# Kernel tuning notes

Measured on AMD Instinct MI355X. Metric: run time of the kernel, lower is better.

Reference implementation:

```python
import jax, jax.numpy as jnp
import numpy as np

N = 20000
E = 320000
F_IN = 256
HID = 32
HEADS = 8
EDGE_DIM = HID // 4  # 8
NEG_SLOPE = 0.2


def _gat_conv(x, src, dst, e_emb, W, att_s, att_d, W_e, att_e, bias, H, C):
    """PyG-style GATConv with edge_dim, add_self_loops=True (fill_value='mean'), concat heads."""
    n = x.shape[0]
    loop = jnp.arange(n, dtype=src.dtype)
    # self-loop edge_attr = scatter-mean of edge_attr by dst (0 for isolated nodes)
    deg = jax.ops.segment_sum(jnp.ones_like(dst, dtype=x.dtype), dst, num_segments=n)
    e_mean = jax.ops.segment_sum(e_emb, dst, num_segments=n) / jnp.maximum(deg, 1.0)[:, None]
    src_a = jnp.concatenate([src, loop])
    dst_a = jnp.concatenate([dst, loop])
    e_all = jnp.concatenate([e_emb, e_mean], axis=0)  # [E+N, edge_dim]

    h = (x @ W).reshape(n, H, C)                      # [N,H,C]
    a_src = jnp.einsum('nhc,hc->nh', h, att_s)        # [N,H]
    a_dst = jnp.einsum('nhc,hc->nh', h, att_d)
    he = (e_all @ W_e).reshape(-1, H, C)              # [E+N,H,C]
    a_edge = jnp.einsum('ehc,hc->eh', he, att_e)      # [E+N,H]

    alpha = jax.nn.leaky_relu(a_src[src_a] + a_dst[dst_a] + a_edge, NEG_SLOPE)
    # segment softmax over destination nodes
    amax = jax.ops.segment_max(alpha, dst_a, num_segments=n)
    alpha = jnp.exp(alpha - amax[dst_a])
    denom = jax.ops.segment_sum(alpha, dst_a, num_segments=n)
    alpha = alpha / (denom[dst_a] + 1e-16)

    msg = h[src_a] * alpha[:, :, None]                # [E+N,H,C]
    out = jax.ops.segment_sum(msg, dst_a, num_segments=n)  # [N,H,C]
    return out.reshape(n, H * C) + bias


def setup_inputs() -> dict:
    key = jax.random.key(0)
    ks = jax.random.split(key, 16)

    def glorot(k, shape):
        fan_in, fan_out = shape[0], shape[-1]
        s = np.sqrt(6.0 / (fan_in + fan_out))
        return jax.random.uniform(k, shape, jnp.float32, -s, s)

    x = jax.random.normal(ks[0], (N, F_IN), jnp.float32)
    edge_index = jax.random.randint(ks[1], (2, E), 0, N, jnp.int32)
    edge_attr = jax.random.uniform(ks[2], (E, 2), jnp.float32)

    # spatial_embed: Linear(2 -> EDGE_DIM)
    Wse = glorot(ks[3], (2, EDGE_DIM))
    bse = jnp.zeros((EDGE_DIM,), jnp.float32)
    # conv1: in=F_IN, heads=HEADS, out=HID, edge_dim=EDGE_DIM
    W1 = glorot(ks[4], (F_IN, HEADS * HID))
    as1 = glorot(ks[5], (HEADS, HID))
    ad1 = glorot(ks[6], (HEADS, HID))
    We1 = glorot(ks[7], (EDGE_DIM, HEADS * HID))
    ae1 = glorot(ks[8], (HEADS, HID))
    b1 = jnp.zeros((HEADS * HID,), jnp.float32)
    # conv2: in=HEADS*HID, heads=1, out=HID
    W2 = glorot(ks[9], (HEADS * HID, HID))
    as2 = glorot(ks[10], (1, HID))
    ad2 = glorot(ks[11], (1, HID))
    We2 = glorot(ks[12], (EDGE_DIM, HID))
    ae2 = glorot(ks[13], (1, HID))
    b2 = jnp.zeros((HID,), jnp.float32)

    return {"x": x, "edge_index": edge_index, "edge_attr": edge_attr,
            "Wse": Wse, "bse": bse,
            "W1": W1, "as1": as1, "ad1": ad1, "We1": We1, "ae1": ae1, "b1": b1,
            "W2": W2, "as2": as2, "ad2": ad2, "We2": We2, "ae2": ae2, "b2": b2}


def reference(x, edge_index, edge_attr, Wse, bse,
              W1, as1, ad1, We1, ae1, b1,
              W2, as2, ad2, We2, ae2, b2):
    src, dst = edge_index[0], edge_index[1]
    e = jax.nn.relu(edge_attr @ Wse + bse)            # [E, EDGE_DIM]
    h = _gat_conv(x, src, dst, e, W1, as1, ad1, We1, ae1, b1, HEADS, HID)
    h = jax.nn.relu(h)                                # dropout inactive (eval)
    out = _gat_conv(h, src, dst, e, W2, as2, ad2, We2, ae2, b2, 1, HID)
    return out
```

## Files before the change

### kernel.cpp

```cpp
#include <hip/hip_runtime.h>
#include <hip/hip_bf16.h>
#include <hip/hip_fp16.h>
#include <float.h>


typedef short v8s __attribute__((ext_vector_type(8)));
typedef float v4f __attribute__((ext_vector_type(4)));

#define WSYNC() do { __asm__ volatile("" ::: "memory"); __builtin_amdgcn_wave_barrier(); } while (0)

__device__ __forceinline__ ushort f2bf(float f) {
  unsigned u = __float_as_uint(f);
  u = (u + 0x7FFF + ((u >> 16) & 1)) >> 16;
  return (ushort)u;
}
__device__ __forceinline__ float bf2f(ushort h) {
  return __uint_as_float(((unsigned)h) << 16);
}
__device__ __forceinline__ unsigned pk2bf(float lo, float hi) {
  return (unsigned)f2bf(lo) | ((unsigned)f2bf(hi) << 16);
}
__device__ __forceinline__ unsigned pk2h(float lo, float hi) {
  return (unsigned)__half_as_ushort(__float2half(lo)) |
         ((unsigned)__half_as_ushort(__float2half(hi)) << 16);
}

__global__ __launch_bounds__(256) void k_pre(const int* __restrict__ dst,
                                             const float* __restrict__ W1,
                                             const float* __restrict__ We1,
                                             const float* __restrict__ ae1,
                                             const float* __restrict__ We2,
                                             const float* __restrict__ ae2,
                                             const float* __restrict__ W2,
                                             int* __restrict__ deg,
                                             ushort* __restrict__ Bt,
                                             float* __restrict__ M1,
                                             float* __restrict__ m2,
                                             float* __restrict__ W2B,
                                             int E, int DB) {
  int b = blockIdx.x;
  if (b < DB) {
    int e = b * 256 + threadIdx.x;
    if (e < E) atomicAdd(&deg[dst[e]], 1);
    return;
  }
  if (b == DB + 64) {
    int t = threadIdx.x;
    for (int i = t; i < 8192; i += 256) {
      int k = i >> 5, cc = i & 31;
      W2B[(size_t)(k >> 2) * 128 + cc * 4 + (k & 3)] = W2[(size_t)k * 32 + cc];
    }
    if (t < 64) {
      int k = t >> 3, h = t & 7;
      float s = 0.f;
      for (int c = 0; c < 32; c++) s += We1[k * 256 + h * 32 + c] * ae1[h * 32 + c];
      M1[k * 8 + h] = s;
    } else if (t < 72) {
      int k = t - 64;
      float s = 0.f;
      for (int c = 0; c < 32; c++) s += We2[k * 32 + c] * ae2[c];
      m2[k] = s;
    }
    return;
  }
  int b2 = b - DB;
  __shared__ float tile[32][33];
  int bx = b2 & 7, by = b2 >> 3;
  int tx = threadIdx.x & 31, ty = threadIdx.x >> 5;
  for (int r = ty; r < 32; r += 8)
    tile[r][tx] = W1[(size_t)(by * 32 + r) * 256 + bx * 32 + tx];
  __syncthreads();
  for (int r = ty; r < 32; r += 8)
    Bt[(size_t)(bx * 32 + r) * 256 + by * 32 + tx] = f2bf(tile[tx][r]);
}

__global__ __launch_bounds__(1024) void k_scan(const int* __restrict__ deg,
                                               int* __restrict__ row_ptr,
                                               int* __restrict__ cursor, int N) {
  __shared__ int part[1024];
  int tid = threadIdx.x;
  int chunk = (N + 1023) / 1024;
  int lo = tid * chunk;
  if (lo > N) lo = N;
  int hi = lo + chunk;
  if (hi > N) hi = N;
  int s = 0;
  for (int i = lo; i < hi; i++) { s += deg[i]; cursor[i] = 0; }
  part[tid] = s;
  __syncthreads();
  for (int off = 1; off < 1024; off <<= 1) {
    int v = 0;
    if (tid >= off) v = part[tid - off];
    __syncthreads();
    part[tid] += v;
    __syncthreads();
  }
  int base = part[tid] - s;
  for (int i = lo; i < hi; i++) { row_ptr[i] = base; base += deg[i]; }
  if (tid == 1023) row_ptr[N] = part[1023];
}

__global__ __launch_bounds__(256) void k_mega1(
    const float* __restrict__ A, const ushort* __restrict__ Bt,
    const float* __restrict__ as1, const float* __restrict__ ad1,
    ushort* __restrict__ h1b, float* __restrict__ asv, float* __restrict__ adv, int M,
    const int* __restrict__ src, const int* __restrict__ dst,
    const float* __restrict__ ea, const float* __restrict__ Wse,
    const float* __restrict__ bse, const float* __restrict__ M1,
    const float* __restrict__ m2, const int* __restrict__ row_ptr,
    int* __restrict__ cursor, char* __restrict__ rec, int E, int GB) {
  __shared__ __align__(16) char smem[27648];
  int t = threadIdx.x;
  if (blockIdx.x >= GB) {
    float* sW  = (float*)smem;
    float* sbv = sW + 16;
    float* sM  = sbv + 8;
    float* sm2 = sM + 64;
    if (t < 16) sW[t] = Wse[t];
    if (t < 8) sbv[t] = bse[t];
    if (t < 64) sM[t] = M1[t];
    if (t >= 64 && t < 72) sm2[t - 64] = m2[t - 64];
    __syncthreads();
    int i = (blockIdx.x - GB) * 256 + t;
    if (i >= E) return;
    float2 av = ((const float2*)ea)[i];
    float e8[8];
#pragma unroll
    for (int k = 0; k < 8; k++)
      e8[k] = fmaxf(av.x * sW[k] + av.y * sW[8 + k] + sbv[k], 0.f);
    float o[8];
#pragma unroll
    for (int h = 0; h < 8; h++) {
      float s = 0.f;
#pragma unroll
      for (int k = 0; k < 8; k++) s += e8[k] * sM[k * 8 + h];
      o[h] = s;
    }
    float s2 = 0.f;
#pragma unroll
    for (int k = 0; k < 8; k++) s2 += e8[k] * sm2[k];
    int d = dst[i];
    int pos = row_ptr[d] + atomicAdd(&cursor[d], 1);
    uint4 w0, w1;
    w0.x = (unsigned)src[i];
    w0.y = pk2h(o[0], o[1]);
    w0.z = pk2h(o[2], o[3]);
    w0.w = pk2h(o[4], o[5]);
    w1.x = pk2h(o[6], o[7]);
    w1.y = __float_as_uint(s2);
    w1.z = 0; w1.w = 0;
    *(uint4*)(rec + (size_t)pos * 32)      = w0;
    *(uint4*)(rec + (size_t)pos * 32 + 16) = w1;
    return;
  }
  ushort* sA = (ushort*)smem;
  ushort* sB = (ushort*)(smem + 5120);
  float* sas = (float*)(smem + 25600);
  float* sad = (float*)(smem + 26624);
  int wave = t >> 6, lane = t & 63;
  int m0 = blockIdx.x * 64;
  int c = lane & 15, kg = lane >> 4;
  sas[t] = as1[t];
  sad[t] = ad1[t];
  v4f acc[4][4];
#pragma unroll
  for (int a = 0; a < 4; a++)
#pragma unroll
    for (int b = 0; b < 4; b++) acc[a][b] = (v4f)(0.f);
  int arow = t >> 2;
  int akoff = (t & 3) * 8;
  bool aval = (m0 + arow) < M;
  const float* aptr = A + (size_t)(m0 + arow) * 256 + akoff;
  const ushort* bptr = Bt + (size_t)t * 256;
  for (int k0 = 0; k0 < 256; k0 += 32) {
    float4 v0 = make_float4(0.f, 0.f, 0.f, 0.f), v1 = v0;
    if (aval) { v0 = *(const float4*)(aptr + k0); v1 = *(const float4*)(aptr + k0 + 4); }
    unsigned* dst32 = (unsigned*)&sA[arow * 40 + akoff];
    dst32[0] = pk2bf(v0.x, v0.y);
    dst32[1] = pk2bf(v0.z, v0.w);
    dst32[2] = pk2bf(v1.x, v1.y);
    dst32[3] = pk2bf(v1.z, v1.w);
    *(v8s*)&sB[t * 40 + 0]  = *(const v8s*)(bptr + k0 + 0);
    *(v8s*)&sB[t * 40 + 8]  = *(const v8s*)(bptr + k0 + 8);
    *(v8s*)&sB[t * 40 + 16] = *(const v8s*)(bptr + k0 + 16);
    *(v8s*)&sB[t * 40 + 24] = *(const v8s*)(bptr + k0 + 24);
    __syncthreads();
    v8s af[4], bfr[4];
#pragma unroll
    for (int mt = 0; mt < 4; mt++) af[mt] = *(v8s*)&sA[(mt * 16 + c) * 40 + kg * 8];
#pragma unroll
    for (int nt = 0; nt < 4; nt++) bfr[nt] = *(v8s*)&sB[(wave * 64 + nt * 16 + c) * 40 + kg * 8];
#pragma unroll
    for (int mt = 0; mt < 4; mt++)
#pragma unroll
      for (int nt = 0; nt < 4; nt++)
        acc[mt][nt] = __builtin_amdgcn_mfma_f32_16x16x32_bf16(af[mt], bfr[nt], acc[mt][nt], 0, 0, 0);
    __syncthreads();
  }
  int colbase = wave * 64;
#pragma unroll
  for (int mt = 0; mt < 4; mt++) {
#pragma unroll
    for (int i = 0; i < 4; i++) {
      int m = m0 + mt * 16 + kg * 4 + i;
      if (m < M) {
#pragma unroll
        for (int nt = 0; nt < 4; nt++)
          h1b[(size_t)m * 256 + colbase + nt * 16 + c] = f2bf(acc[mt][nt][i]);
      }
      float s1a = acc[mt][0][i] * sas[colbase + c]      + acc[mt][1][i] * sas[colbase + 16 + c];
      float s2a = acc[mt][0][i] * sad[colbase + c]      + acc[mt][1][i] * sad[colbase + 16 + c];
      float s1b = acc[mt][2][i] * sas[colbase + 32 + c] + acc[mt][3][i] * sas[colbase + 48 + c];
      float s2b = acc[mt][2][i] * sad[colbase + 32 + c] + acc[mt][3][i] * sad[colbase + 48 + c];
#pragma unroll
      for (int o = 1; o < 16; o <<= 1) {
        s1a += __shfl_xor(s1a, o);
        s2a += __shfl_xor(s2a, o);
        s1b += __shfl_xor(s1b, o);
        s2b += __shfl_xor(s2b, o);
      }
      if (c == 0 && m < M) {
        asv[(size_t)m * 8 + 2 * wave]     = s1a;
        adv[(size_t)m * 8 + 2 * wave]     = s2a;
        asv[(size_t)m * 8 + 2 * wave + 1] = s1b;
        adv[(size_t)m * 8 + 2 * wave + 1] = s2b;
      }
    }
  }
}

__global__ __launch_bounds__(256) void k_conv1(
    const int* __restrict__ row_ptr, const char* __restrict__ rec,
    const float* __restrict__ asv, const float* __restrict__ adv,
    const ushort* __restrict__ h1b, const float* __restrict__ b1,
    const float* __restrict__ W2B, const float* __restrict__ as2,
    const float* __restrict__ ad2, float* __restrict__ g2,
    float* __restrict__ asv2, float* __restrict__ adv2, int N) {
  __shared__ float sw_all[4][64 * 8];
  __shared__ int ssrc_all[4][64];
  __shared__ float sm_all[4][8], sl_all[4][8], sadv_all[4][8], smean_all[4][8];
  __shared__ float sh2_all[4][256];
  int wid = threadIdx.x >> 6;
  int lane = threadIdx.x & 63;
  int n = blockIdx.x * 4 + wid;
  if (n >= N) return;
  float* sw = sw_all[wid];
  int* ssrc = ssrc_all[wid];
  float* sm = sm_all[wid];
  float* sl = sl_all[wid];
  float* sadv = sadv_all[wid];
  float* smean = smean_all[wid];
  float* sh2 = sh2_all[wid];
  int h = lane >> 3;
  int sub = lane & 7;
  int hh = lane & 7;
  int begin = row_ptr[n], end = row_ptr[n + 1];
  int degr = end - begin;
  if (lane < 8) { sm[lane] = -FLT_MAX; sl[lane] = 0.f; sadv[lane] = adv[(size_t)n * 8 + lane]; }
  WSYNC();
  float aedsum = 0.f;
  float4 acc = make_float4(0.f, 0.f, 0.f, 0.f);
  for (int cs = begin; cs < end; cs += 64) {
    int c = min(64, end - cs);
    WSYNC();
    if (lane < c) ssrc[lane] = *(const int*)(rec + (size_t)(cs + lane) * 32);
    WSYNC();
    for (int idx = lane; idx < c * 8; idx += 64) {
      int el = idx >> 3;
      float ae = __half2float(*(const __half*)(rec + (size_t)(cs + el) * 32 + 4 + hh * 2));
      aedsum += ae;
      float a = asv[(size_t)ssrc[el] * 8 + hh] + sadv[hh] + ae;
      a = a > 0.f ? a : 0.2f * a;
      sw[idx] = a;
    }
    WSYNC();
    float mloc = -FLT_MAX;
    for (int el = sub; el < c; el += 8) mloc = fmaxf(mloc, sw[el * 8 + h]);
#pragma unroll
    for (int o = 1; o < 8; o <<= 1) mloc = fmaxf(mloc, __shfl_xor(mloc, o));
    float mold = sm[h];
    float mnew = fmaxf(mold, mloc);
    float scale = __expf(mold - mnew);
    float lloc = 0.f;
    for (int el = sub; el < c; el += 8) {
      float w = __expf(sw[el * 8 + h] - mnew);
      sw[el * 8 + h] = w;
      lloc += w;
    }
#pragma unroll
    for (int o = 1; o < 8; o <<= 1) lloc += __shfl_xor(lloc, o);
    WSYNC();
    if (sub == 0) { sm[h] = mnew; sl[h] = sl[h] * scale + lloc; }
    acc.x *= scale; acc.y *= scale; acc.z *= scale; acc.w *= scale;
#pragma unroll 2
    for (int el = 0; el < c; el++) {
      float w = sw[el * 8 + h];
      ushort4 hv = *(const ushort4*)(h1b + (size_t)ssrc[el] * 256 + lane * 4);
      acc.x += w * bf2f(hv.x);
      acc.y += w * bf2f(hv.y);
      acc.z += w * bf2f(hv.z);
      acc.w += w * bf2f(hv.w);
    }
  }
  aedsum += __shfl_xor(aedsum, 8);
  aedsum += __shfl_xor(aedsum, 16);
  aedsum += __shfl_xor(aedsum, 32);
  float invd = 1.f / (float)(degr > 1 ? degr : 1);
  if (lane < 8) smean[lane] = aedsum * invd;
  WSYNC();
  float a_self = asv[(size_t)n * 8 + h] + sadv[h] + smean[h];
  a_self = a_self > 0.f ? a_self : 0.2f * a_self;
  float mold = sm[h];
  float mnew = fmaxf(mold, a_self);
  float scale = __expf(mold - mnew);
  float w_self = __expf(a_self - mnew);
  float l_fin = sl[h] * scale + w_self;
  ushort4 hs = *(const ushort4*)(h1b + (size_t)n * 256 + lane * 4);
  acc.x = acc.x * scale + w_self * bf2f(hs.x);
  acc.y = acc.y * scale + w_self * bf2f(hs.y);
  acc.z = acc.z * scale + w_self * bf2f(hs.z);
  acc.w = acc.w * scale + w_self * bf2f(hs.w);
  float inv = 1.f / (l_fin + 1e-16f);
  float4 bv = *(const float4*)(b1 + lane * 4);
  float4 h2v;
  h2v.x = fmaxf(acc.x * inv + bv.x, 0.f);
  h2v.y = fmaxf(acc.y * inv + bv.y, 0.f);
  h2v.z = fmaxf(acc.z * inv + bv.z, 0.f);
  h2v.w = fmaxf(acc.w * inv + bv.w, 0.f);
  *(float4*)&sh2[lane * 4] = h2v;
  WSYNC();
  int half = lane >> 5, cc = lane & 31;
  const float* wp = W2B + (size_t)half * 32 * 128 + cc * 4;
  const float* hp2 = sh2 + half * 128;
  float part = 0.f;
#pragma unroll 8
  for (int g = 0; g < 32; g++) {
    float4 wv = *(const float4*)(wp + g * 128);
    float4 hv = *(const float4*)(hp2 + g * 4);
    part += wv.x * hv.x + wv.y * hv.y + wv.z * hv.z + wv.w * hv.w;
  }
  part += __shfl_xor(part, 32);
  float s1 = part * as2[cc];
  float s2 = part * ad2[cc];
#pragma unroll
  for (int o = 1; o < 32; o <<= 1) {
    s1 += __shfl_xor(s1, o);
    s2 += __shfl_xor(s2, o);
  }
  if (lane < 32) g2[(size_t)n * 32 + cc] = part;
  if (lane == 0) { asv2[n] = s1; adv2[n] = s2; }
}

__global__ __launch_bounds__(256) void k_conv2(
    const int* __restrict__ row_ptr, const char* __restrict__ rec,
    const float* __restrict__ asv2, const float* __restrict__ adv2,
    const float* __restrict__ g2, const float* __restrict__ b2,
    float* __restrict__ out, int N) {
  __shared__ float sw_all[4][64];
  __shared__ int ssrc_all[4][64];
  int wid = threadIdx.x >> 6;
  int lane = threadIdx.x & 63;
  int n = blockIdx.x * 4 + wid;
  if (n >= N) return;
  float* sw = sw_all[wid];
  int* ssrc = ssrc_all[wid];
  int sub = lane >> 3, q = lane & 7;
  int begin = row_ptr[n], end = row_ptr[n + 1];
  int degr = end - begin;
  float advn = adv2[n];
  float m = -FLT_MAX, l = 0.f, aedsum = 0.f;
  float4 acc = make_float4(0.f, 0.f, 0.f, 0.f);
  for (int cs = begin; cs < end; cs += 64) {
    int c = min(64, end - cs);
    WSYNC();
    float a = -FLT_MAX;
    if (lane < c) {
      const char* rp = rec + (size_t)(cs + lane) * 32;
      int s = *(const int*)rp;
      ssrc[lane] = s;
      float ae = *(const float*)(rp + 20);
      aedsum += ae;
      a = asv2[s] + advn + ae;
      a = a > 0.f ? a : 0.2f * a;
    }
    float cm = a;
#pragma unroll
    for (int o = 1; o < 64; o <<= 1) cm = fmaxf(cm, __shfl_xor(cm, o));
    float nm = fmaxf(m, cm);
    float sc = __expf(m - nm);
    float w = (lane < c) ? __expf(a - nm) : 0.f;
    float cl = w;
#pragma unroll
    for (int o = 1; o < 64; o <<= 1) cl += __shfl_xor(cl, o);
    l = l * sc + cl;
    m = nm;
    sw[lane] = w;
    WSYNC();
    acc.x *= sc; acc.y *= sc; acc.z *= sc; acc.w *= sc;
#pragma unroll 2
    for (int el = sub; el < c; el += 8) {
      float w2 = sw[el];
      const float4 gv = *(const float4*)(g2 + (size_t)ssrc[el] * 32 + q * 4);
      acc.x += w2 * gv.x; acc.y += w2 * gv.y; acc.z += w2 * gv.z; acc.w += w2 * gv.w;
    }
  }
#pragma unroll
  for (int o = 1; o < 64; o <<= 1) aedsum += __shfl_xor(aedsum, o);
  float invd = 1.f / (float)(degr > 1 ? degr : 1);
  float a_self = asv2[n] + advn + aedsum * invd;
  a_self = a_self > 0.f ? a_self : 0.2f * a_self;
  float nm = fmaxf(m, a_self);
  float sc = __expf(m - nm);
  float w_self = __expf(a_self - nm);
  l = l * sc + w_self;
  acc.x *= sc; acc.y *= sc; acc.z *= sc; acc.w *= sc;
  if (sub == 0) {
    const float4 gv = *(const float4*)(g2 + (size_t)n * 32 + q * 4);
    acc.x += w_self * gv.x; acc.y += w_self * gv.y;
    acc.z += w_self * gv.z; acc.w += w_self * gv.w;
  }
#pragma unroll
  for (int o = 8; o < 64; o <<= 1) {
    acc.x += __shfl_xor(acc.x, o);
    acc.y += __shfl_xor(acc.y, o);
    acc.z += __shfl_xor(acc.z, o);
    acc.w += __shfl_xor(acc.w, o);
  }
  if (lane < 8) {
    float inv = 1.f / (l + 1e-16f);
    float4 bv = *(const float4*)(b2 + lane * 4);
    float4 o4;
    o4.x = acc.x * inv + bv.x;
    o4.y = acc.y * inv + bv.y;
    o4.z = acc.z * inv + bv.z;
    o4.w = acc.w * inv + bv.w;
    *(float4*)(out + (size_t)n * 32 + lane * 4) = o4;
  }
}

extern "C" void kernel_launch(void* const* d_in, const int* in_sizes, int n_in,
                              void* d_out, int out_size, void* d_ws, size_t ws_size,
                              hipStream_t stream) {
  (void)n_in; (void)out_size; (void)ws_size;
  const float* x   = (const float*)d_in[0];
  const int*   ei  = (const int*)d_in[1];
  const float* ea  = (const float*)d_in[2];
  const float* Wse = (const float*)d_in[3];
  const float* bse = (const float*)d_in[4];
  const float* W1  = (const float*)d_in[5];
  const float* as1 = (const float*)d_in[6];
  const float* ad1 = (const float*)d_in[7];
  const float* We1 = (const float*)d_in[8];
  const float* ae1 = (const float*)d_in[9];
  const float* b1  = (const float*)d_in[10];
  const float* W2  = (const float*)d_in[11];
  const float* as2 = (const float*)d_in[12];
  const float* ad2 = (const float*)d_in[13];
  const float* We2 = (const float*)d_in[14];
  const float* ae2 = (const float*)d_in[15];
  const float* b2  = (const float*)d_in[16];
  const int N = in_sizes[0] / 256;
  const int E = in_sizes[1] / 2;
  const int* src = ei;
  const int* dst = ei + E;

  char* base = (char*)d_ws;
  size_t off = 0;
  auto alloc = [&](size_t bytes) -> char* {
    off = (off + 255) & ~(size_t)255;
    char* p = base + off;
    off += bytes;
    return p;
  };
  int*   deg      = (int*)alloc((size_t)N * 4);
  int*   cursor   = (int*)alloc((size_t)N * 4);
  int* row_ptr    = (int*)alloc((size_t)(N + 1) * 4);
  char* rec       = alloc((size_t)E * 32);
  ushort* W1T     = (ushort*)alloc((size_t)256 * 256 * 2);
  float* W2B      = (float*)alloc((size_t)256 * 32 * 4);
  ushort* h1b     = (ushort*)alloc((size_t)N * 256 * 2);
  float* asv1     = (float*)alloc((size_t)N * 8 * 4);
  float* adv1     = (float*)alloc((size_t)N * 8 * 4);
  float* g2       = (float*)alloc((size_t)N * 32 * 4);
  float* asv2     = (float*)alloc((size_t)N * 4);
  float* adv2     = (float*)alloc((size_t)N * 4);
  float* M1       = (float*)alloc(64 * 4);
  float* m2       = (float*)alloc(8 * 4);

  const int DB = (E + 255) / 256;
  const int GB = (N + 63) / 64;
  hipMemsetAsync(deg, 0, (size_t)N * 4, stream);
  k_pre<<<DB + 65, 256, 0, stream>>>(dst, W1, We1, ae1, We2, ae2, W2,
                                     deg, W1T, M1, m2, W2B, E, DB);
  k_scan<<<1, 1024, 0, stream>>>(deg, row_ptr, cursor, N);
  k_mega1<<<GB + DB, 256, 0, stream>>>(x, W1T, as1, ad1, h1b, asv1, adv1, N,
                                       src, dst, ea, Wse, bse, M1, m2, row_ptr,
                                       cursor, rec, E, GB);
  k_conv1<<<(N + 3) / 4, 256, 0, stream>>>(row_ptr, rec, asv1, adv1, h1b, b1,
                                           W2B, as2, ad2, g2, asv2, adv2, N);
  k_conv2<<<(N + 3) / 4, 256, 0, stream>>>(row_ptr, rec, asv2, adv2, g2, b2,
                                           (float*)d_out, N);
}
```

Baseline: 233.6 us.

## Replace LDS staging with register wave shuffles in GAT aggregation kernels

Both conv aggregation kernels stop staging source ids, attention weights and softmax state in shared memory guarded by wave barriers. That data now stays in registers and is broadcast with cross-lane shuffles, and the gather loop in conv1 is fully unrolled over 64 edges with per-edge guards. The aim is to cut LDS traffic and barrier stalls on the per-edge critical path. In exchange it raises register pressure and shuffle count, and the fully unrolled loop still runs its guard checks on low-degree chunks.

After: 275.9 us. +18.1%, slower.

```diff
diff --git a/kernel.cpp b/kernel.cpp
--- a/kernel.cpp
+++ b/kernel.cpp
@@ -236,85 +236,90 @@
     const float* __restrict__ W2B, const float* __restrict__ as2,
     const float* __restrict__ ad2, float* __restrict__ g2,
     float* __restrict__ asv2, float* __restrict__ adv2, int N) {
-  __shared__ float sw_all[4][64 * 8];
-  __shared__ int ssrc_all[4][64];
-  __shared__ float sm_all[4][8], sl_all[4][8], sadv_all[4][8], smean_all[4][8];
   __shared__ float sh2_all[4][256];
   int wid = threadIdx.x >> 6;
   int lane = threadIdx.x & 63;
   int n = blockIdx.x * 4 + wid;
   if (n >= N) return;
-  float* sw = sw_all[wid];
-  int* ssrc = ssrc_all[wid];
-  float* sm = sm_all[wid];
-  float* sl = sl_all[wid];
-  float* sadv = sadv_all[wid];
-  float* smean = smean_all[wid];
   float* sh2 = sh2_all[wid];
   int h = lane >> 3;
-  int sub = lane & 7;
+  int rgrp = lane >> 3;
   int hh = lane & 7;
   int begin = row_ptr[n], end = row_ptr[n + 1];
   int degr = end - begin;
-  if (lane < 8) { sm[lane] = -FLT_MAX; sl[lane] = 0.f; sadv[lane] = adv[(size_t)n * 8 + lane]; }
-  WSYNC();
-  float aedsum = 0.f;
+  float advn = adv[(size_t)n * 8 + hh];
+  float m_run = -FLT_MAX, l_run = 0.f, aedsum = 0.f;
   float4 acc = make_float4(0.f, 0.f, 0.f, 0.f);
   for (int cs = begin; cs < end; cs += 64) {
     int c = min(64, end - cs);
-    WSYNC();
-    if (lane < c) ssrc[lane] = *(const int*)(rec + (size_t)(cs + lane) * 32);
-    WSYNC();
-    for (int idx = lane; idx < c * 8; idx += 64) {
-      int el = idx >> 3;
-      float ae = __half2float(*(const __half*)(rec + (size_t)(cs + el) * 32 + 4 + hh * 2));
-      aedsum += ae;
-      float a = asv[(size_t)ssrc[el] * 8 + hh] + sadv[hh] + ae;
-      a = a > 0.f ? a : 0.2f * a;
-      sw[idx] = a;
-    }
-    WSYNC();
+    int srcid = 0;
+    if (lane < c) srcid = *(const int*)(rec + (size_t)(cs + lane) * 32);
+    float wreg[8];
     float mloc = -FLT_MAX;
-    for (int el = sub; el < c; el += 8) mloc = fmaxf(mloc, sw[el * 8 + h]);
-#pragma unroll
-    for (int o = 1; o < 8; o <<= 1) mloc = fmaxf(mloc, __shfl_xor(mloc, o));
-    float mold = sm[h];
-    float mnew = fmaxf(mold, mloc);
-    float scale = __expf(mold - mnew);
+#pragma unroll
+    for (int j = 0; j < 8; j++) {
+      int el = j * 8 + rgrp;
+      int se = __shfl(srcid, el);
+      float a = -FLT_MAX;
+      if (el < c) {
+        float ae = __half2float(*(const __half*)(rec + (size_t)(cs + el) * 32 + 4 + hh * 2));
+        aedsum += ae;
+        a = asv[(size_t)se * 8 + hh] + advn + ae;
+        a = a > 0.f ? a : 0.2f * a;
+      }
+      wreg[j] = a;
+      mloc = fmaxf(mloc, a);
+    }
+    mloc = fmaxf(mloc, __shfl_xor(mloc, 8));
+    mloc = fmaxf(mloc, __shfl_xor(mloc, 16));
+    mloc = fmaxf(mloc, __shfl_xor(mloc, 32));
+    float mnew = fmaxf(m_run, mloc);
+    float scale = __expf(m_run - mnew);
     float lloc = 0.f;
-    for (int el = sub; el < c; el += 8) {
-      float w = __expf(sw[el * 8 + h] - mnew);
-      sw[el * 8 + h] = w;
+#pragma unroll
+    for (int j = 0; j < 8; j++) {
+      int el = j * 8 + rgrp;
+      float w = (el < c) ? __expf(wreg[j] - mnew) : 0.f;
+      wreg[j] = w;
       lloc += w;
     }
-#pragma unroll
-    for (int o = 1; o < 8; o <<= 1) lloc += __shfl_xor(lloc, o);
-    WSYNC();
-    if (sub == 0) { sm[h] = mnew; sl[h] = sl[h] * scale + lloc; }
-    acc.x *= scale; acc.y *= scale; acc.z *= scale; acc.w *= scale;
-#pragma unroll 2
-    for (int el = 0; el < c; el++) {
-      float w = sw[el * 8 + h];
-      ushort4 hv = *(const ushort4*)(h1b + (size_t)ssrc[el] * 256 + lane * 4);
-      acc.x += w * bf2f(hv.x);
-      acc.y += w * bf2f(hv.y);
-      acc.z += w * bf2f(hv.z);
-      acc.w += w * bf2f(hv.w);
+    lloc += __shfl_xor(lloc, 8);
+    lloc += __shfl_xor(lloc, 16);
+    lloc += __shfl_xor(lloc, 32);
+    l_run = l_run * scale + lloc;
+    m_run = mnew;
+    float sc_h = __shfl(scale, h);
+    acc.x *= sc_h; acc.y *= sc_h; acc.z *= sc_h; acc.w *= sc_h;
+#pragma unroll
+    for (int j = 0; j < 8; j++) {
+#pragma unroll
+      for (int e8 = 0; e8 < 8; e8++) {
+        int el = j * 8 + e8;
+        if (el < c) {
+          int se = __shfl(srcid, el);
+          float w = __shfl(wreg[j], (e8 << 3) | h);
+          ushort4 hv = *(const ushort4*)(h1b + (size_t)se * 256 + lane * 4);
+          acc.x += w * bf2f(hv.x);
+          acc.y += w * bf2f(hv.y);
+          acc.z += w * bf2f(hv.z);
+          acc.w += w * bf2f(hv.w);
+        }
+      }
     }
   }
   aedsum += __shfl_xor(aedsum, 8);
   aedsum += __shfl_xor(aedsum, 16);
   aedsum += __shfl_xor(aedsum, 32);
   float invd = 1.f / (float)(degr > 1 ? degr : 1);
-  if (lane < 8) smean[lane] = aedsum * invd;
-  WSYNC();
-  float a_self = asv[(size_t)n * 8 + h] + sadv[h] + smean[h];
+  float mean_h = __shfl(aedsum, h) * invd;
+  float m_h = __shfl(m_run, h);
+  float l_h = __shfl(l_run, h);
+  float a_self = asv[(size_t)n * 8 + h] + adv[(size_t)n * 8 + h] + mean_h;
   a_self = a_self > 0.f ? a_self : 0.2f * a_self;
-  float mold = sm[h];
-  float mnew = fmaxf(mold, a_self);
-  float scale = __expf(mold - mnew);
+  float mnew = fmaxf(m_h, a_self);
+  float scale = __expf(m_h - mnew);
   float w_self = __expf(a_self - mnew);
-  float l_fin = sl[h] * scale + w_self;
+  float l_fin = l_h * scale + w_self;
   ushort4 hs = *(const ushort4*)(h1b + (size_t)n * 256 + lane * 4);
   acc.x = acc.x * scale + w_self * bf2f(hs.x);
   acc.y = acc.y * scale + w_self * bf2f(hs.y);
@@ -356,14 +361,10 @@
     const float* __restrict__ asv2, const float* __restrict__ adv2,
     const float* __restrict__ g2, const float* __restrict__ b2,
     float* __restrict__ out, int N) {
-  __shared__ float sw_all[4][64];
-  __shared__ int ssrc_all[4][64];
   int wid = threadIdx.x >> 6;
   int lane = threadIdx.x & 63;
   int n = blockIdx.x * 4 + wid;
   if (n >= N) return;
-  float* sw = sw_all[wid];
-  int* ssrc = ssrc_all[wid];
   int sub = lane >> 3, q = lane & 7;
   int begin = row_ptr[n], end = row_ptr[n + 1];
   int degr = end - begin;
@@ -372,15 +373,14 @@
   float4 acc = make_float4(0.f, 0.f, 0.f, 0.f);
   for (int cs = begin; cs < end; cs += 64) {
     int c = min(64, end - cs);
-    WSYNC();
+    int srcid = 0;
     float a = -FLT_MAX;
     if (lane < c) {
       const char* rp = rec + (size_t)(cs + lane) * 32;
-      int s = *(const int*)rp;
-      ssrc[lane] = s;
+      srcid = *(const int*)rp;
       float ae = *(const float*)(rp + 20);
       aedsum += ae;
-      a = asv2[s] + advn + ae;
+      a = asv2[srcid] + advn + ae;
       a = a > 0.f ? a : 0.2f * a;
     }
     float cm = a;
@@ -394,14 +394,16 @@
     for (int o = 1; o < 64; o <<= 1) cl += __shfl_xor(cl, o);
     l = l * sc + cl;
     m = nm;
-    sw[lane] = w;
-    WSYNC();
     acc.x *= sc; acc.y *= sc; acc.z *= sc; acc.w *= sc;
-#pragma unroll 2
-    for (int el = sub; el < c; el += 8) {
-      float w2 = sw[el];
-      const float4 gv = *(const float4*)(g2 + (size_t)ssrc[el] * 32 + q * 4);
-      acc.x += w2 * gv.x; acc.y += w2 * gv.y; acc.z += w2 * gv.z; acc.w += w2 * gv.w;
+    int kmax = (c + 7) >> 3;
+    for (int k = 0; k < kmax; k++) {
+      int el = k * 8 + sub;
+      float w2 = __shfl(w, el);
+      int se = __shfl(srcid, el);
+      if (el < c) {
+        const float4 gv = *(const float4*)(g2 + (size_t)se * 32 + q * 4);
+        acc.x += w2 * gv.x; acc.y += w2 * gv.y; acc.z += w2 * gv.z; acc.w += w2 * gv.w;
+      }
     }
   }
 #pragma unroll
```
